# Kernel tuning notes

Measured on AMD Instinct MI355X. Metric: run time of the kernel, lower is better.

Reference implementation:

```python
import jax, jax.numpy as jnp
import numpy as np

BETA = 0.25

def setup_inputs() -> dict:
    key = jax.random.key(0)
    k1, k2 = jax.random.split(key)
    z = jax.random.normal(k1, (32, 1024, 256), dtype=jnp.float32)
    codebook = jax.random.uniform(k2, (256, 8192), dtype=jnp.float32)  # (code_dim, num_codes)
    return {"z": z, "codebook": codebook}

def reference(z, codebook):
    code_dim = codebook.shape[0]
    z_flat = z.reshape(-1, code_dim)                                   # [N, D]
    # squared-distance matrix: ||z||^2 - 2 z@C + ||c||^2  -> [N, K]
    d = (jnp.sum(z_flat ** 2, axis=1, keepdims=True)
         - 2.0 * jnp.dot(z_flat, codebook)
         + jnp.sum(codebook ** 2, axis=0, keepdims=True))
    indices = jnp.argmin(d, axis=1)                                    # [N]
    z_q = codebook.T[indices].reshape(z.shape)                         # gather codes
    commitment_loss = BETA * jnp.mean((jax.lax.stop_gradient(z_q) - z) ** 2)
    codebook_loss = jnp.mean((z_q - jax.lax.stop_gradient(z)) ** 2)
    z_q_ste = z + jax.lax.stop_gradient(z_q - z)                       # straight-through
    loss = commitment_loss + codebook_loss
    return z_q_ste, indices.reshape(z.shape[:-1]), loss
```

## Files before the change

### kernel.cpp

```cpp
#include <hip/hip_runtime.h>
#include <hip/hip_bf16.h>
#include <stdint.h>


#define DEVINL __device__ __forceinline__

typedef int   intx4 __attribute__((ext_vector_type(4)));

#define NROWS   32768
#define DIMS    256
#define NCODES  8192
#define KMIN    ((int)0x80000000)

DEVINL int q8(float v, float s) {
  int q = __float2int_rn(v * s);
  return min(127, max(-127, q));
}
DEVINL unsigned pk4(float4 v, float s) {
  int a = q8(v.x, s), b = q8(v.y, s), c = q8(v.z, s), d = q8(v.w, s);
  return (unsigned)(a & 255) | ((unsigned)(b & 255) << 8) |
         ((unsigned)(c & 255) << 16) | ((unsigned)(d & 255) << 24);
}
DEVINL void gload_lds16(const void* g, void* lds) {
  __builtin_amdgcn_global_load_lds(
      (const __attribute__((address_space(1))) uint32_t*)(uintptr_t)g,
      (__attribute__((address_space(3))) uint32_t*)(uint32_t)(uintptr_t)lds,
      16, 0, 0);
}

__global__ void k_nrm(const float* __restrict__ cb, int* __restrict__ nrm) {
  __shared__ int p[256];
  int j = blockIdx.x * 32 + (threadIdx.x & 31);
  int seg = threadIdx.x >> 5;
  int s = 0;
  for (int i = 0; i < 32; ++i) {
    int q = q8(cb[(size_t)(seg * 32 + i) * NCODES + j], 127.0f);
    s += q * q;
  }
  p[threadIdx.x] = s;
  __syncthreads();
  if (threadIdx.x < 32) {
    int t = 0;
    for (int k = 0; k < 8; ++k) t += p[k * 32 + threadIdx.x];
    nrm[j] = (int)rintf((25.0f / 254.0f) * (float)t);
  }
}

__global__ void k_transpose(const float* __restrict__ cb, float* __restrict__ cbTf) {
  __shared__ float t[64][65];
  int j0 = blockIdx.x * 64, d0 = blockIdx.y * 64;
  int tx = threadIdx.x & 63, ty = threadIdx.x >> 6;
  #pragma unroll
  for (int i = 0; i < 16; ++i) {
    int dl = i * 4 + ty;
    t[dl][tx] = cb[(size_t)(d0 + dl) * NCODES + j0 + tx];
  }
  __syncthreads();
  #pragma unroll
  for (int i = 0; i < 16; ++i) {
    int jl = i * 4 + ty;
    cbTf[(size_t)(j0 + jl) * DIMS + d0 + tx] = t[tx][jl];
  }
}

__global__ void k_image(const float* __restrict__ cbTf, uint4* __restrict__ img) {
  int g = blockIdx.x * 256 + threadIdx.x;
  int step = g >> 11;
  int r = g & 2047;
  int wc = r >> 9, cf = (r >> 6) & 7, lgr = (r >> 4) & 3, l15 = r & 15;
  int tile = step >> 2, chunk = step & 3;
  int j = tile * 512 + wc * 128 + cf * 16 + l15;
  int d = chunk * 64 + lgr * 16;
  const float4* s4 = (const float4*)(cbTf + (size_t)j * DIMS + d);
  uint4 o;
  o.x = pk4(s4[0], 127.0f); o.y = pk4(s4[1], 127.0f);
  o.z = pk4(s4[2], 127.0f); o.w = pk4(s4[3], 127.0f);
  img[g] = o;
}

__global__ __launch_bounds__(512, 4)
void k_scan(const float* __restrict__ z, const int* __restrict__ nrm,
            const uint4* __restrict__ img, int2* __restrict__ cand) {
  __shared__ char smem[81920];
  char* const zb = smem;
  char* const bb = smem + 16384;

  const int t = threadIdx.x;
  const int lane = t & 63;
  const int wave = t >> 6;
  const int wgr = wave >> 2;
  const int wc  = wave & 3;
  const int l15 = lane & 15;
  const int lgr = lane >> 4;
  const int brow = blockIdx.x * 64;

  #pragma unroll
  for (int i = 0; i < 2; ++i) {
    int g = t + i * 512;
    int row = g >> 4, kb = g & 15;
    const float4* src = (const float4*)(z + (size_t)(brow + row) * DIMS + kb * 16);
    uint4 o;
    o.x = pk4(src[0], 25.0f); o.y = pk4(src[1], 25.0f);
    o.z = pk4(src[2], 25.0f); o.w = pk4(src[3], 25.0f);
    int addr = row * 256 + ((kb * 16) ^ ((row & 15) << 4));
    *(uint4*)(zb + addr) = o;
  }
  {
    const uint4* gsrc = img + wave * 64 + lane;
    #pragma unroll
    for (int i = 0; i < 4; ++i)
      gload_lds16(gsrc + i * 512, bb + (i * 512 + wave * 64) * 16);
  }

  int k1[8], k2[8];
  #pragma unroll
  for (int i = 0; i < 8; ++i) { k1[i] = KMIN; k2[i] = KMIN; }

  __syncthreads();

  intx4 acc[2][8];

  #pragma unroll 1
  for (int s = 0; s < 64; ++s) {
    const int tile = s >> 2, chunk = s & 3;

    if (s > 0) {
      asm volatile("s_waitcnt vmcnt(0)" ::: "memory");
      __builtin_amdgcn_s_barrier();
    }
    if (s < 63) {
      const uint4* gsrc = img + (size_t)(s + 1) * 2048 + wave * 64 + lane;
      char* dst = bb + ((s + 1) & 1) * 32768;
      #pragma unroll
      for (int i = 0; i < 4; ++i)
        gload_lds16(gsrc + i * 512, dst + (i * 512 + wave * 64) * 16);
    }

    const char* cbuf = bb + (s & 1) * 32768;

    if (chunk == 0) {
      #pragma unroll
      for (int cf = 0; cf < 8; ++cf) {
        int h = -nrm[tile * 512 + wc * 128 + cf * 16 + l15];
        acc[0][cf] = intx4{h, h, h, h};
        acc[1][cf] = intx4{h, h, h, h};
      }
    }

    intx4 a[2];
    #pragma unroll
    for (int rf = 0; rf < 2; ++rf) {
      int m = wgr * 32 + rf * 16 + l15;
      int by = (chunk * 64 + lgr * 16) ^ (l15 << 4);
      a[rf] = *(const intx4*)(zb + m * 256 + by);
    }
    #pragma unroll
    for (int cf = 0; cf < 8; ++cf) {
      intx4 b = *(const intx4*)(cbuf + (wc * 512 + cf * 64 + lane) * 16);
      acc[0][cf] = __builtin_amdgcn_mfma_i32_16x16x64_i8(a[0], b, acc[0][cf], 0, 0, 0);
      acc[1][cf] = __builtin_amdgcn_mfma_i32_16x16x64_i8(a[1], b, acc[1][cf], 0, 0, 0);
    }

    if (chunk == 3) {
      const int jinvb = 8191 - (tile * 512 + wc * 128 + l15);
      #pragma unroll
      for (int rf = 0; rf < 2; ++rf)
        #pragma unroll
        for (int cf = 0; cf < 8; ++cf) {
          int jinv = jinvb - cf * 16;
          #pragma unroll
          for (int r = 0; r < 4; ++r) {
            int si = rf * 4 + r;
            int k = ((acc[rf][cf][r] >> 5) << 13) + jinv;
            int t1 = max(k1[si], k);
            int t2 = min(k1[si], k);
            k1[si] = t1;
            k2[si] = max(k2[si], t2);
          }
        }
    }
  }

  #pragma unroll
  for (int rf = 0; rf < 2; ++rf)
    #pragma unroll
    for (int r = 0; r < 4; ++r) {
      int row = brow + wgr * 32 + rf * 16 + lgr * 4 + r;
      int si = rf * 4 + r;
      cand[(size_t)row * 64 + wc * 16 + l15] = make_int2(k1[si], k2[si]);
    }
}

__global__ __launch_bounds__(512)
void k_refine(const float* __restrict__ z, const float* __restrict__ cbTf,
              const int2* __restrict__ cand, float* __restrict__ zq,
              float* __restrict__ oidx, double* __restrict__ parts) {
  __shared__ double lsum[8];
  int lane = threadIdx.x & 63, wave = threadIdx.x >> 6;
  int row = blockIdx.x * 8 + wave;

  float4 z4 = ((const float4*)(z + (size_t)row * DIMS))[lane];
  int2 kp = cand[(size_t)row * 64 + lane];
  int ka = kp.x, kb = kp.y;

  double bd = 1e300; int bj = -1; float4 bc = {0.f, 0.f, 0.f, 0.f};
  for (int s = 0; s < 5; ++s) {
    int km = max(ka, kb);
    #pragma unroll
    for (int m = 1; m < 64; m <<= 1) km = max(km, __shfl_xor(km, m, 64));
    int j = 8191 - (km & 8191);
    if (ka == km) ka = KMIN; else if (kb == km) kb = KMIN;

    float4 c4 = ((const float4*)(cbTf + (size_t)j * DIMS))[lane];
    double dx = (double)z4.x - (double)c4.x;
    double dy = (double)z4.y - (double)c4.y;
    double dzv = (double)z4.z - (double)c4.z;
    double dw = (double)z4.w - (double)c4.w;
    double d = dx * dx + dy * dy + dzv * dzv + dw * dw;
    #pragma unroll
    for (int m = 1; m < 64; m <<= 1) d += __shfl_xor(d, m, 64);

    bool bt = (d < bd) || (d == bd && j < bj);
    if (bt) { bd = d; bj = j; bc = c4; }
  }

  ((float4*)(zq + (size_t)row * DIMS))[lane] = bc;
  if (lane == 0) oidx[row] = (float)bj;

  double lx = (double)bc.x - (double)z4.x;
  double ly = (double)bc.y - (double)z4.y;
  double lz = (double)bc.z - (double)z4.z;
  double lw = (double)bc.w - (double)z4.w;
  double l = lx * lx + ly * ly + lz * lz + lw * lw;
  #pragma unroll
  for (int m = 1; m < 64; m <<= 1) l += __shfl_xor(l, m, 64);
  if (lane == 0) lsum[wave] = l;
  __syncthreads();
  if (threadIdx.x == 0) {
    double s = 0;
    for (int i = 0; i < 8; ++i) s += lsum[i];
    parts[blockIdx.x] = s;
  }
}

__global__ void k_finish(const double* __restrict__ parts, float* __restrict__ out) {
  __shared__ double s[256];
  double a = 0;
  for (int i = threadIdx.x; i < 4096; i += 256) a += parts[i];
  s[threadIdx.x] = a;
  __syncthreads();
  for (int w = 128; w; w >>= 1) {
    if (threadIdx.x < w) s[threadIdx.x] += s[threadIdx.x + w];
    __syncthreads();
  }
  if (threadIdx.x == 0) out[0] = (float)(1.25 * s[0] / 8388608.0);
}

extern "C" void kernel_launch(void* const* d_in, const int* in_sizes, int n_in,
                              void* d_out, int out_size, void* d_ws, size_t ws_size,
                              hipStream_t stream) {
  const float* zin = (const float*)d_in[0];
  const float* cb  = (const float*)d_in[1];
  float* out = (float*)d_out;

  char* w = (char*)d_ws;
  int*    nrm   = (int*)w;
  float*  cbTf  = (float*)(w + 32768);
  char*   imgb  = w + 32768 + 8388608;
  int2*   cand  = (int2*)(w + 32768 + 8388608 + 2097152);
  double* parts = (double*)(w + 32768 + 8388608 + 2097152 + 16777216);

  float* zq_out   = out;
  float* idx_out  = out + 8388608;
  float* loss_out = out + 8388608 + 32768;

  k_nrm<<<dim3(256), dim3(256), 0, stream>>>(cb, nrm);
  k_transpose<<<dim3(128, 4), dim3(256), 0, stream>>>(cb, cbTf);
  k_image<<<dim3(512), dim3(256), 0, stream>>>(cbTf, (uint4*)imgb);
  k_scan<<<dim3(512), dim3(512), 0, stream>>>(zin, nrm, (const uint4*)imgb, cand);
  k_refine<<<dim3(4096), dim3(512), 0, stream>>>(zin, cbTf, cand, zq_out, idx_out, parts);
  k_finish<<<dim3(1), dim3(256), 0, stream>>>(parts, loss_out);
}
```

Before: 163.6 us.

## Double-buffer scan accumulators to overlap top-2 fold with next tile MFMAs

Splits the accumulators into two ping-pong sets so the top-2 reduction (shift/max/min fold) for the previous codebook tile runs during chunks 1-2 of the next tile, interleaved with its MFMAs instead of serializing after chunk 3. The chunk loop is fully unrolled per tile, and a tail fold handles the last tile. Launch bounds drop from 4 to 2 waves-per-EU minimum to allow the doubled accumulator register footprint. This lowers occupancy in exchange for better overlap of VALU and MFMA work.

```diff
diff --git a/kernel.cpp b/kernel.cpp
--- a/kernel.cpp
+++ b/kernel.cpp
@@ -78,7 +78,7 @@
   img[g] = o;
 }
 
-__global__ __launch_bounds__(512, 4)
+__global__ __launch_bounds__(512, 2)
 void k_scan(const float* __restrict__ z, const int* __restrict__ nrm,
             const uint4* __restrict__ img, int2* __restrict__ cand) {
   __shared__ char smem[81920];
@@ -118,67 +118,94 @@
 
   __syncthreads();
 
-  intx4 acc[2][8];
-
-  #pragma unroll 1
-  for (int s = 0; s < 64; ++s) {
-    const int tile = s >> 2, chunk = s & 3;
-
-    if (s > 0) {
-      asm volatile("s_waitcnt vmcnt(0)" ::: "memory");
-      __builtin_amdgcn_s_barrier();
-    }
-    if (s < 63) {
-      const uint4* gsrc = img + (size_t)(s + 1) * 2048 + wave * 64 + lane;
-      char* dst = bb + ((s + 1) & 1) * 32768;
-      #pragma unroll
-      for (int i = 0; i < 4; ++i)
-        gload_lds16(gsrc + i * 512, dst + (i * 512 + wave * 64) * 16);
-    }
-
-    const char* cbuf = bb + (s & 1) * 32768;
-
-    if (chunk == 0) {
+  intx4 accA[2][8], accB[2][8];
+
+  auto tbody = [&](int tileIdx, intx4 (&cur)[2][8], intx4 (&prv)[2][8],
+                   bool doFold) {
+    #pragma unroll
+    for (int chunk = 0; chunk < 4; ++chunk) {
+      const int s = tileIdx * 4 + chunk;
+      if (s > 0) {
+        asm volatile("s_waitcnt vmcnt(0)" ::: "memory");
+        __builtin_amdgcn_s_barrier();
+      }
+      if (s < 63) {
+        const uint4* gsrc = img + (size_t)(s + 1) * 2048 + wave * 64 + lane;
+        char* dst = bb + ((s + 1) & 1) * 32768;
+        #pragma unroll
+        for (int i = 0; i < 4; ++i)
+          gload_lds16(gsrc + i * 512, dst + (i * 512 + wave * 64) * 16);
+      }
+      const char* cbuf = bb + (s & 1) * 32768;
+
+      if (chunk == 0) {
+        #pragma unroll
+        for (int cf = 0; cf < 8; ++cf) {
+          int h = -nrm[tileIdx * 512 + wc * 128 + cf * 16 + l15];
+          cur[0][cf] = intx4{h, h, h, h};
+          cur[1][cf] = intx4{h, h, h, h};
+        }
+      }
+
+      intx4 a0, a1;
+      {
+        int by = (chunk * 64 + lgr * 16) ^ (l15 << 4);
+        a0 = *(const intx4*)(zb + (wgr * 32 + l15) * 256 + by);
+        a1 = *(const intx4*)(zb + (wgr * 32 + 16 + l15) * 256 + by);
+      }
       #pragma unroll
       for (int cf = 0; cf < 8; ++cf) {
-        int h = -nrm[tile * 512 + wc * 128 + cf * 16 + l15];
-        acc[0][cf] = intx4{h, h, h, h};
-        acc[1][cf] = intx4{h, h, h, h};
+        intx4 b = *(const intx4*)(cbuf + (wc * 512 + cf * 64 + lane) * 16);
+        cur[0][cf] = __builtin_amdgcn_mfma_i32_16x16x64_i8(a0, b, cur[0][cf], 0, 0, 0);
+        cur[1][cf] = __builtin_amdgcn_mfma_i32_16x16x64_i8(a1, b, cur[1][cf], 0, 0, 0);
+      }
+
+      if (doFold && (chunk == 1 || chunk == 2)) {
+        const int jb = 8191 - ((tileIdx - 1) * 512 + wc * 128 + l15);
+        #pragma unroll
+        for (int rf = 0; rf < 2; ++rf)
+          #pragma unroll
+          for (int co = 0; co < 4; ++co) {
+            const int cf = (chunk - 1) * 4 + co;
+            const int jinv = jb - cf * 16;
+            #pragma unroll
+            for (int r = 0; r < 4; ++r) {
+              const int si = rf * 4 + r;
+              int kk = ((prv[rf][cf][r] >> 5) << 13) + jinv;
+              int u1 = max(k1[si], kk);
+              int u2 = min(k1[si], kk);
+              k1[si] = u1;
+              k2[si] = max(k2[si], u2);
+            }
+          }
       }
     }
-
-    intx4 a[2];
-    #pragma unroll
-    for (int rf = 0; rf < 2; ++rf) {
-      int m = wgr * 32 + rf * 16 + l15;
-      int by = (chunk * 64 + lgr * 16) ^ (l15 << 4);
-      a[rf] = *(const intx4*)(zb + m * 256 + by);
-    }
-    #pragma unroll
-    for (int cf = 0; cf < 8; ++cf) {
-      intx4 b = *(const intx4*)(cbuf + (wc * 512 + cf * 64 + lane) * 16);
-      acc[0][cf] = __builtin_amdgcn_mfma_i32_16x16x64_i8(a[0], b, acc[0][cf], 0, 0, 0);
-      acc[1][cf] = __builtin_amdgcn_mfma_i32_16x16x64_i8(a[1], b, acc[1][cf], 0, 0, 0);
-    }
-
-    if (chunk == 3) {
-      const int jinvb = 8191 - (tile * 512 + wc * 128 + l15);
+  };
+
+  tbody(0, accA, accB, false);
+  tbody(1, accB, accA, true);
+  #pragma unroll 1
+  for (int tp = 1; tp < 8; ++tp) {
+    tbody(2 * tp,     accA, accB, true);
+    tbody(2 * tp + 1, accB, accA, true);
+  }
+  {
+    const int jb = 8191 - (15 * 512 + wc * 128 + l15);
+    #pragma unroll
+    for (int rf = 0; rf < 2; ++rf)
       #pragma unroll
-      for (int rf = 0; rf < 2; ++rf)
+      for (int cf = 0; cf < 8; ++cf) {
+        const int jinv = jb - cf * 16;
         #pragma unroll
-        for (int cf = 0; cf < 8; ++cf) {
-          int jinv = jinvb - cf * 16;
-          #pragma unroll
-          for (int r = 0; r < 4; ++r) {
-            int si = rf * 4 + r;
-            int k = ((acc[rf][cf][r] >> 5) << 13) + jinv;
-            int t1 = max(k1[si], k);
-            int t2 = min(k1[si], k);
-            k1[si] = t1;
-            k2[si] = max(k2[si], t2);
-          }
+        for (int r = 0; r < 4; ++r) {
+          const int si = rf * 4 + r;
+          int kk = ((accB[rf][cf][r] >> 5) << 13) + jinv;
+          int u1 = max(k1[si], kk);
+          int u2 = min(k1[si], kk);
+          k1[si] = u1;
+          k2[si] = max(k2[si], u2);
         }
-    }
+      }
   }
 
   #pragma unroll
```

Result: slower. 236.8 us (+44.7%).
